# Performance work log

Hardware: AMD Instinct MI355X
Metric: run time of the kernel (lower is better)

The kernel has to match this reference:

```python
import jax, jax.numpy as jnp
import numpy as np

B, T, D, V, LMAX = 16, 512, 256, 4233, 64
NEG = -1e30  # finite 'log zero' keeps grads NaN-free


def setup_inputs() -> dict:
    key = jax.random.key(0)
    k1, k2, k3, k4 = jax.random.split(key, 4)
    hs_pad = jax.random.normal(k1, (B, T, D), dtype=jnp.float32)
    hlens = jnp.full((B,), T, dtype=jnp.int32)
    ys_pad = jax.random.randint(k2, (B, LMAX), 1, V, dtype=jnp.int32)  # blank=0 excluded
    ys_lens = jax.random.randint(k3, (B,), LMAX // 2, LMAX + 1, dtype=jnp.int32)
    W = jax.random.normal(k4, (V, D), dtype=jnp.float32) * (1.0 / np.sqrt(D))
    b = jnp.zeros((V,), dtype=jnp.float32)
    return {"hs_pad": hs_pad, "hlens": hlens, "ys_pad": ys_pad,
            "ys_lens": ys_lens, "W": W, "b": b}


def _ctc_loss_sum(logp_tbv, ext, allow, hlens, ys_lens):
    """logp_tbv: [T,B,V] log-softmax; ext: [B,S] extended labels (blank-interleaved).
    Returns sum over batch of -log p(y|x) (torch CTCLoss reduction='sum')."""
    Tn, Bn, _ = logp_tbv.shape
    S = ext.shape[1]
    # per-frame log-prob of each extended label: [T,B,S]
    lp_ext = jnp.take_along_axis(
        logp_tbv, jnp.broadcast_to(ext[None], (Tn, Bn, S)), axis=2)

    # t = 0 init: alpha[0]=lp(blank), alpha[1]=lp(y_1)
    alpha0 = jnp.full((Bn, S), NEG, dtype=logp_tbv.dtype)
    alpha0 = alpha0.at[:, 0].set(lp_ext[0, :, 0])
    alpha0 = alpha0.at[:, 1].set(lp_ext[0, :, 1])

    def step(alpha, inp):
        lp_t, t = inp  # lp_t: [B,S]
        a1 = jnp.pad(alpha[:, :-1], ((0, 0), (1, 0)), constant_values=NEG)
        a2 = jnp.pad(alpha[:, :-2], ((0, 0), (2, 0)), constant_values=NEG)
        a2 = jnp.where(allow, a2, NEG)
        new = jnp.logaddexp(jnp.logaddexp(alpha, a1), a2) + lp_t
        alpha = jnp.where((t < hlens)[:, None], new, alpha)  # freeze past hlen
        return alpha, None

    ts = jnp.arange(1, Tn, dtype=jnp.int32)
    alpha, _ = jax.lax.scan(step, alpha0, (lp_ext[1:], ts))

    last = 2 * ys_lens  # index of final blank state
    bi = jnp.arange(Bn)
    ll = jnp.logaddexp(alpha[bi, last], alpha[bi, last - 1])
    return -jnp.sum(ll)


def reference(hs_pad, hlens, ys_pad, ys_lens, W, b):
    # linear projection + log_softmax (dropout_rate=0.0 -> identity)
    logits = jnp.einsum('btd,vd->btv', hs_pad, W) + b
    logp = jax.nn.log_softmax(logits, axis=-1)          # [B,T,V]
    logp = jnp.transpose(logp, (1, 0, 2))               # [T,B,V]

    Bn, Lmax = ys_pad.shape
    S = 2 * Lmax + 1
    ext = jnp.zeros((Bn, S), dtype=ys_pad.dtype).at[:, 1::2].set(ys_pad)
    prev2 = jnp.pad(ext, ((0, 0), (2, 0)))[:, :-2]
    allow = (ext != 0) & (ext != prev2) & (jnp.arange(S) >= 2)

    loss = _ctc_loss_sum(logp, ext, allow, hlens, ys_lens)
    return loss / Bn  # module divides by ys_hat.size(1) == batch
```

## Files before the change

### kernel.cpp

```cpp
#include <hip/hip_runtime.h>

constexpr int Bn = 16;
constexpr int Tn = 512;
constexpr int Dn = 256;
constexpr int Vn = 4233;
constexpr int Vp = 4352;
constexpr int Ln = 64;
constexpr int Un = 80;
constexpr int CS = 68;
constexpr int NCB = 34;
constexpr int Mtot = Bn * Tn;

#define LN2     0.6931471805599453f
#define INV_LN2 1.4426950408889634f

typedef __attribute__((ext_vector_type(8))) short short8;
typedef __attribute__((ext_vector_type(4))) float f32x4;

__device__ __forceinline__ float lg2(float x) { return __builtin_amdgcn_logf(x); }
__device__ __forceinline__ float ex2(float x) { return __builtin_amdgcn_exp2f(x); }

__device__ __forceinline__ unsigned short cvt_bf16(float f) {
    unsigned int u = __float_as_uint(f);
    u = (u + 0x7fffu + ((u >> 16) & 1u)) >> 16;
    return (unsigned short)u;
}

__device__ __forceinline__ void gl_lds16(const void* g, void* l) {
    __builtin_amdgcn_global_load_lds(
        (const __attribute__((address_space(1))) void*)g,
        (__attribute__((address_space(3))) void*)l,
        16, 0, 0);
}

__device__ __forceinline__ double dpp_shr1_d(double v) {
    union { double d; int i[2]; } u, r;
    u.d = v;
    r.i[0] = __builtin_amdgcn_update_dpp(0, u.i[0], 0x138, 0xF, 0xF, false);
    r.i[1] = __builtin_amdgcn_update_dpp(0, u.i[1], 0x138, 0xF, 0xF, false);
    return r.d;
}

__device__ __forceinline__ int wave_imax(int v) {
    int t;
    t = __builtin_amdgcn_update_dpp(v, v, 0xB1,  0xF, 0xF, false); v = (t > v) ? t : v;
    t = __builtin_amdgcn_update_dpp(v, v, 0x4E,  0xF, 0xF, false); v = (t > v) ? t : v;
    t = __builtin_amdgcn_update_dpp(v, v, 0x141, 0xF, 0xF, false); v = (t > v) ? t : v;
    t = __builtin_amdgcn_update_dpp(v, v, 0x140, 0xF, 0xF, false); v = (t > v) ? t : v;
    int a = __builtin_amdgcn_readlane(v, 0);
    int b = __builtin_amdgcn_readlane(v, 16);
    int c = __builtin_amdgcn_readlane(v, 32);
    int d = __builtin_amdgcn_readlane(v, 48);
    int ab = (a > b) ? a : b;
    int cd = (c > d) ? c : d;
    return (ab > cd) ? ab : cd;
}

__global__ __launch_bounds__(256) void conv(
    const float* __restrict__ hs, const float* __restrict__ W,
    const float* __restrict__ bias, const int* __restrict__ ys,
    unsigned short* __restrict__ hs_b, unsigned short* __restrict__ w_b,
    float* __restrict__ gbias, float* __restrict__ out)
{
    const int gid = blockIdx.x * 256 + threadIdx.x;
    const int stride = gridDim.x * 256;
    const float4* hs4 = (const float4*)hs;
    const float4* W4  = (const float4*)W;

    if (gid == 0) out[0] = 0.0f;

    for (int i = gid; i < (Bn * Tn * Dn) / 4; i += stride) {
        float4 v = hs4[i];
        ushort4 o = make_ushort4(cvt_bf16(v.x), cvt_bf16(v.y), cvt_bf16(v.z), cvt_bf16(v.w));
        *(ushort4*)(&hs_b[i * 4]) = o;
    }
    for (int i = gid; i < Vp * (Dn / 4); i += stride) {
        int row = i >> 6;
        float4 v = make_float4(0.f, 0.f, 0.f, 0.f);
        if (row < Vn) v = W4[i];
        ushort4 o = make_ushort4(cvt_bf16(v.x), cvt_bf16(v.y), cvt_bf16(v.z), cvt_bf16(v.w));
        *(ushort4*)(&w_b[i * 4]) = o;
    }
    for (int i = gid; i < Bn * 128; i += stride) {
        int b = i >> 7;
        int u = i & 127;
        int v = (u == 0) ? 0 : ((u <= Ln) ? ys[b * Ln + u - 1] : -1);
        gbias[i] = (v >= 0) ? bias[v] : 0.0f;
    }
}

__global__ __launch_bounds__(256) void gemm_se(
    const unsigned short* __restrict__ hs_b, const unsigned short* __restrict__ w_b,
    const int* __restrict__ ys, const float* __restrict__ bias,
    const float* __restrict__ gbias, float* __restrict__ sep,
    float* __restrict__ glg2)
{
    __shared__ __align__(16) short lsA[128 * 64];
    __shared__ __align__(16) short lsB[128 * 64];

    const int tid = threadIdx.x;
    const int lane = tid & 63;
    const int w = tid >> 6;
    const int lr = lane & 15;
    const int kq = lane >> 4;
    const int m0 = blockIdx.x * 128;
    const int mw = w * 32;
    const bool gather = (blockIdx.y == NCB);
    const int b = blockIdx.x >> 2;

    const int srow = lane >> 3;
    const int scg  = (lane & 7) ^ (srow & 7);
    const int scol = scg * 8;

    const unsigned short* bptr[4];
    #pragma unroll
    for (int j = 0; j < 4; ++j) {
        int c = w * 4 + j;
        int row = c * 8 + srow;
        int v;
        if (gather) {
            if (row == 0) v = 0;
            else if (row <= Ln) v = ys[b * Ln + row - 1];
            else v = Vn + 32;
        } else {
            v = blockIdx.y * 128 + row;
        }
        bptr[j] = w_b + (size_t)v * Dn + scol;
    }

    f32x4 acc[2][8];
    #pragma unroll
    for (int mf = 0; mf < 2; ++mf)
        #pragma unroll
        for (int nf = 0; nf < 8; ++nf)
            acc[mf][nf] = (f32x4){0.f, 0.f, 0.f, 0.f};

    for (int ks = 0; ks < 4; ++ks) {
        const int k0 = ks * 64;
        __syncthreads();
        #pragma unroll
        for (int j = 0; j < 4; ++j) {
            int c = w * 4 + j;
            int row = c * 8 + srow;
            gl_lds16(hs_b + (size_t)(m0 + row) * Dn + k0 + scol, (char*)lsA + c * 1024);
            gl_lds16(bptr[j] + k0,                               (char*)lsB + c * 1024);
        }
        __syncthreads();

        #pragma unroll
        for (int sub = 0; sub < 2; ++sub) {
            short8 af[2], bf[8];
            #pragma unroll
            for (int mf = 0; mf < 2; ++mf) {
                int row = mw + mf * 16 + lr;
                int cg = (sub * 4 + kq) ^ (row & 7);
                af[mf] = *(const short8*)(&lsA[row * 64 + cg * 8]);
            }
            #pragma unroll
            for (int nf = 0; nf < 8; ++nf) {
                int row = nf * 16 + lr;
                int cg = (sub * 4 + kq) ^ (row & 7);
                bf[nf] = *(const short8*)(&lsB[row * 64 + cg * 8]);
            }
            #pragma unroll
            for (int mf = 0; mf < 2; ++mf)
                #pragma unroll
                for (int nf = 0; nf < 8; ++nf)
                    acc[mf][nf] = __builtin_amdgcn_mfma_f32_16x16x32_bf16(
                        af[mf], bf[nf], acc[mf][nf], 0, 0, 0);
        }
    }

    if (!gather) {
        const int n0 = blockIdx.y * 128;
        float bcol[8]; bool valid[8];
        #pragma unroll
        for (int nf = 0; nf < 8; ++nf) {
            int col = n0 + nf * 16 + lr;
            valid[nf] = (col < Vn);
            bcol[nf] = valid[nf] ? bias[col] : 0.0f;
        }
        #pragma unroll
        for (int mf = 0; mf < 2; ++mf) {
            #pragma unroll
            for (int r = 0; r < 4; ++r) {
                float s = 0.0f;
                #pragma unroll
                for (int nf = 0; nf < 8; ++nf)
                    if (valid[nf]) s += __expf(acc[mf][nf][r] + bcol[nf]);
                #pragma unroll
                for (int off = 1; off < 16; off <<= 1) s += __shfl_xor(s, off, 64);
                if (lr == 0)
                    sep[(size_t)blockIdx.y * Mtot + m0 + mw + mf * 16 + kq * 4 + r] = s;
            }
        }
    } else {
        #pragma unroll
        for (int mf = 0; mf < 2; ++mf) {
            #pragma unroll
            for (int nf = 0; nf < 5; ++nf) {
                int u = nf * 16 + lr;
                float gv = gbias[b * 128 + u];
                #pragma unroll
                for (int r = 0; r < 4; ++r) {
                    int g = m0 + mw + mf * 16 + kq * 4 + r;
                    glg2[(size_t)g * Un + u] = (acc[mf][nf][r] + gv) * INV_LN2;
                }
            }
        }
    }
}

__global__ __launch_bounds__(256) void ctc_fwd(
    const float* __restrict__ pmat, const float* __restrict__ sep,
    const int* __restrict__ ys, const int* __restrict__ hlens,
    const int* __restrict__ ylens, float* __restrict__ out)
{
    __shared__ __align__(16) union SMem {
        struct {
            float ls[2][64 * CS + 4];
            double shO[64], shE[64], shZ[64];
            int   shX[64];
        } c;
        struct { float wsum[4]; } r;
    } sm;

    const int tid = threadIdx.x;
    const int l = tid & 63;
    const int w = tid >> 6;

    if (blockIdx.x >= 16) {
        const int b = blockIdx.x - 16;
        const int hl = hlens[b];
        float corrAcc = 0.0f;
        #pragma unroll
        for (int j = 0; j < 2; ++j) {
            int t = tid + j * 256;
            float s = 0.0f;
            #pragma unroll
            for (int c = 0; c < NCB; ++c)
                s += sep[(size_t)c * Mtot + b * Tn + t];
            if (t < hl) corrAcc += lg2(s);
        }
        #pragma unroll
        for (int off = 1; off < 64; off <<= 1) corrAcc += __shfl_xor(corrAcc, off, 64);
        if (l == 0) sm.r.wsum[w] = corrAcc;
        __syncthreads();
        if (tid == 0)
            atomicAdd(out, (sm.r.wsum[0] + sm.r.wsum[1] + sm.r.wsum[2] + sm.r.wsum[3])
                           * (LN2 / (float)Bn));
        return;
    }

    const int b = blockIdx.x;
    const int hl = hlens[b];
    int yl  = ys[b * Ln + l];
    int ylm = (l >= 1) ? ys[b * Ln + l - 1] : -1;
    const double aF = ((l >= 1) && (yl != ylm)) ? 1.0 : 0.0;

    const float* pm = pmat + (size_t)b * Tn * Un;

    #pragma unroll
    for (int j = 0; j < 4; ++j) {
        int i = tid + j * 256;
        int tt = i >> 4, u4 = (i & 15) * 4;
        float4 v = *(const float4*)(pm + (size_t)(1 + tt) * Un + u4);
        v.x = ex2(v.x); v.y = ex2(v.y); v.z = ex2(v.z); v.w = ex2(v.w);
        *(float4*)(&sm.c.ls[0][tt * CS + u4]) = v;
    }
    if (tid < 64) sm.c.ls[0][tid * CS + 64] = ex2(pm[(size_t)(1 + tid) * Un + 64]);
    __syncthreads();

    double o = (l == 0) ? (double)ex2(pm[1]) : 0.0;
    double e = (l == 0) ? (double)ex2(pm[0]) : 0.0;
    double z = 0.0;
    int ex = 0;

    float4 r4a = make_float4(0.f,0.f,0.f,0.f), r4b = r4a, r4c = r4a, r4d = r4a;
    float r1 = 0.0f;

    double qa0, qa1, qa2, qa3, ra0, ra1, ra2, ra3;
    double qb0, qb1, qb2, qb3, rb0, rb1, rb2, rb3;
    double qc0, qc1, qc2, qc3, rc0, rc1, rc2, rc3;

#define RENORM32 do { \
        double mm = fmax(fmax(o, e), z); \
        union { double d; unsigned int ui[2]; } um; um.d = mm; \
        int kk = (int)((um.ui[1] >> 20) & 2047u) - 1023; \
        int km = wave_imax(kk); \
        o = ldexp(o, -km); e = ldexp(e, -km); z = ldexp(z, -km); \
        ex += km; \
    } while (0)

#define STEPR(qv, rv) do { \
        double an = dpp_shr1_d(o); \
        double nO = fma(aF, an, o + e) * (rv); \
        double nE = (e + an) * (qv); \
        double nZ = (z + o) * (qv); \
        o = nO; e = nE; z = nZ; \
    } while (0)

#define LDA(base) do { \
        qa0 = (double)buf[(base) * CS];       ra0 = (double)buf[(base) * CS + 1 + l]; \
        qa1 = (double)buf[((base)+1) * CS];   ra1 = (double)buf[((base)+1) * CS + 1 + l]; \
        qa2 = (double)buf[((base)+2) * CS];   ra2 = (double)buf[((base)+2) * CS + 1 + l]; \
        qa3 = (double)buf[((base)+3) * CS];   ra3 = (double)buf[((base)+3) * CS + 1 + l]; \
    } while (0)
#define LDB(base) do { \
        qb0 = (double)buf[(base) * CS];       rb0 = (double)buf[(base) * CS + 1 + l]; \
        qb1 = (double)buf[((base)+1) * CS];   rb1 = (double)buf[((base)+1) * CS + 1 + l]; \
        qb2 = (double)buf[((base)+2) * CS];   rb2 = (double)buf[((base)+2) * CS + 1 + l]; \
        qb3 = (double)buf[((base)+3) * CS];   rb3 = (double)buf[((base)+3) * CS + 1 + l]; \
    } while (0)
#define LDC(base) do { \
        qc0 = (double)buf[(base) * CS];       rc0 = (double)buf[(base) * CS + 1 + l]; \
        qc1 = (double)buf[((base)+1) * CS];   rc1 = (double)buf[((base)+1) * CS + 1 + l]; \
        qc2 = (double)buf[((base)+2) * CS];   rc2 = (double)buf[((base)+2) * CS + 1 + l]; \
        qc3 = (double)buf[((base)+3) * CS];   rc3 = (double)buf[((base)+3) * CS + 1 + l]; \
    } while (0)

#define W4A do { STEPR(qa0,ra0); STEPR(qa1,ra1); STEPR(qa2,ra2); STEPR(qa3,ra3); } while (0)
#define W4B do { STEPR(qb0,rb0); STEPR(qb1,rb1); STEPR(qb2,rb2); STEPR(qb3,rb3); } while (0)
#define W4C do { STEPR(qc0,rc0); STEPR(qc1,rc1); STEPR(qc2,rc2); STEPR(qc3,rc3); } while (0)

#define STEPS(Joff, ACT) do { \
        RENORM32; \
        double q = (double)buf[(Joff) * CS]; \
        double r = (double)buf[(Joff) * CS + 1 + l]; \
        double an = dpp_shr1_d(o); \
        double nO = fma(aF, an, o + e) * r; \
        double nE = (e + an) * q; \
        double nZ = (z + o) * q; \
        bool act = (ACT); \
        o = act ? nO : o; e = act ? nE : e; z = act ? nZ : z; \
    } while (0)

    for (int c = 0; c < 8; ++c) {
        if (c < 7) {
            const int tb = 1 + (c + 1) * 64;
            { int i = tid;       int tt = i >> 4, u4 = (i & 15) * 4;
              r4a = (tb + tt < Tn) ? *(const float4*)(pm + (size_t)(tb + tt) * Un + u4) : make_float4(0.f,0.f,0.f,0.f); }
            { int i = tid + 256; int tt = i >> 4, u4 = (i & 15) * 4;
              r4b = (tb + tt < Tn) ? *(const float4*)(pm + (size_t)(tb + tt) * Un + u4) : make_float4(0.f,0.f,0.f,0.f); }
            { int i = tid + 512; int tt = i >> 4, u4 = (i & 15) * 4;
              r4c = (tb + tt < Tn) ? *(const float4*)(pm + (size_t)(tb + tt) * Un + u4) : make_float4(0.f,0.f,0.f,0.f); }
            { int i = tid + 768; int tt = i >> 4, u4 = (i & 15) * 4;
              r4d = (tb + tt < Tn) ? *(const float4*)(pm + (size_t)(tb + tt) * Un + u4) : make_float4(0.f,0.f,0.f,0.f); }
            if (tid < 64)
                r1 = (tb + tid < Tn) ? pm[(size_t)(tb + tid) * Un + 64] : 0.0f;
        }

        const float* buf = sm.c.ls[c & 1];

        if (c < 7) {
            if (hl >= (c + 1) * 64 + 1) {
                RENORM32;
                LDA(0); LDB(4);
                LDC(8);  W4A;
                LDA(12); W4B;
                LDB(16); W4C;
                LDC(20); W4A;
                LDA(24); W4B;
                LDB(28); W4C;
                LDC(32); W4A;
                LDA(36); W4B;
                RENORM32;
                LDB(40); W4C;
                LDC(44); W4A;
                LDA(48); W4B;
                LDB(52); W4C;
                LDC(56); W4A;
                LDA(60); W4B;
                W4C;
                W4A;
            } else {
                #pragma unroll 1
                for (int j = 0; j < 64; ++j)
                    STEPS(j, (c * 64 + 1 + j) < hl);
            }
        } else {
            if (hl >= Tn) {
                RENORM32;
                LDA(0); LDB(4);
                LDC(8);  W4A;
                LDA(12); W4B;
                LDB(16); W4C;
                LDC(20); W4A;
                LDA(24); W4B;
                LDB(28); W4C;
                LDC(32); W4A;
                LDA(36); W4B;
                RENORM32;
                LDB(40); W4C;
                LDC(44); W4A;
                LDA(48); W4B;
                LDB(52); W4C;
                LDC(56); W4A;
                LDA(60); W4B;
                W4C;
                STEPR(qa0, ra0); STEPR(qa1, ra1); STEPR(qa2, ra2);
            } else {
                #pragma unroll 1
                for (int j = 0; j < 63; ++j)
                    STEPS(j, (449 + j) < hl);
            }
        }

        if (c < 7) {
            const int tb = 1 + (c + 1) * 64;
            float* dst = sm.c.ls[(c + 1) & 1];
            { int i = tid;       int tt = i >> 4, u4 = (i & 15) * 4; float4 v = r4a;
              v.x = ex2(v.x); v.y = ex2(v.y); v.z = ex2(v.z); v.w = ex2(v.w);
              if (tb + tt >= Tn) v = make_float4(0.f,0.f,0.f,0.f);
              *(float4*)(&dst[tt * CS + u4]) = v; }
            { int i = tid + 256; int tt = i >> 4, u4 = (i & 15) * 4; float4 v = r4b;
              v.x = ex2(v.x); v.y = ex2(v.y); v.z = ex2(v.z); v.w = ex2(v.w);
              if (tb + tt >= Tn) v = make_float4(0.f,0.f,0.f,0.f);
              *(float4*)(&dst[tt * CS + u4]) = v; }
            { int i = tid + 512; int tt = i >> 4, u4 = (i & 15) * 4; float4 v = r4c;
              v.x = ex2(v.x); v.y = ex2(v.y); v.z = ex2(v.z); v.w = ex2(v.w);
              if (tb + tt >= Tn) v = make_float4(0.f,0.f,0.f,0.f);
              *(float4*)(&dst[tt * CS + u4]) = v; }
            { int i = tid + 768; int tt = i >> 4, u4 = (i & 15) * 4; float4 v = r4d;
              v.x = ex2(v.x); v.y = ex2(v.y); v.z = ex2(v.z); v.w = ex2(v.w);
              if (tb + tt >= Tn) v = make_float4(0.f,0.f,0.f,0.f);
              *(float4*)(&dst[tt * CS + u4]) = v; }
            if (tid < 64)
                dst[tid * CS + 64] = (tb + tid < Tn) ? ex2(r1) : 0.0f;
        }
        __syncthreads();
    }
#undef RENORM32
#undef STEPR
#undef LDA
#undef LDB
#undef LDC
#undef W4A
#undef W4B
#undef W4C
#undef STEPS

    if (tid < 64) { sm.c.shO[l] = o; sm.c.shE[l] = e; sm.c.shZ[l] = z; sm.c.shX[l] = ex; }
    __syncthreads();

    if (tid == 0) {
        int L = ylens[b];
        double vo = sm.c.shO[L - 1]; int xo = sm.c.shX[L - 1];
        double ve; int xe;
        if (L == 64) { ve = sm.c.shZ[63]; xe = sm.c.shX[63]; }
        else         { ve = sm.c.shE[L];  xe = sm.c.shX[L]; }
        int em = (xo > xe) ? xo : xe;
        double s = ldexp(vo, xo - em) + ldexp(ve, xe - em);
        union { double d; unsigned int ui[2]; } us; us.d = s;
        int ks = (int)((us.ui[1] >> 20) & 2047u) - 1023;
        double mant = ldexp(s, -ks);
        float ll = (lg2((float)mant) + (float)(ks + em)) * LN2;
        atomicAdd(out, -ll / (float)Bn);
    }
}

extern "C" void kernel_launch(void* const* d_in, const int* in_sizes, int n_in,
                              void* d_out, int out_size, void* d_ws, size_t ws_size,
                              hipStream_t stream) {
    const float* hs    = (const float*)d_in[0];
    const int*   hlens = (const int*)d_in[1];
    const int*   ys    = (const int*)d_in[2];
    const int*   ylens = (const int*)d_in[3];
    const float* W     = (const float*)d_in[4];
    const float* bias  = (const float*)d_in[5];
    float* out = (float*)d_out;

    char* ws = (char*)d_ws;
    unsigned short* hs_b = (unsigned short*)(ws);
    unsigned short* w_b  = (unsigned short*)(ws + 4194304);
    float* glg2  = (float*)(ws + 6422528);
    float* sep   = (float*)(ws + 9043968);
    float* gbias = (float*)(ws + 10158080);

    conv<<<1024, 256, 0, stream>>>(hs, W, bias, ys, hs_b, w_b, gbias, out);
    gemm_se<<<dim3(64, NCB + 1), 256, 0, stream>>>(hs_b, w_b, ys, bias, gbias, sep, glg2);
    ctc_fwd<<<32, 256, 0, stream>>>(glg2, sep, ys, hlens, ylens, out);
}
```

Before: 117.4 us.

## Make GEMM persistent with resident A panel and double-buffered B tiles

The GEMM grid changes from 64x35 independent tiles to 256 blocks. Each block loads its full 128x256 hs panel into LDS once, then walks every fourth column tile, double-buffering the W half-tiles so the next load overlaps MFMA work. This removes the repeated reloading of the A panel and the two barriers per k-step. In exchange it uses much more LDS (about 128KB per block at one block per CU) and leaves fewer blocks to hide latency.

Result: slower. 162.2 us (+38.2%).

```diff
diff --git a/kernel.cpp b/kernel.cpp
--- a/kernel.cpp
+++ b/kernel.cpp
@@ -89,44 +89,54 @@
     }
 }
 
-__global__ __launch_bounds__(256) void gemm_se(
+__global__ __launch_bounds__(256, 1) void gemm_se(
     const unsigned short* __restrict__ hs_b, const unsigned short* __restrict__ w_b,
     const int* __restrict__ ys, const float* __restrict__ bias,
     const float* __restrict__ gbias, float* __restrict__ sep,
     float* __restrict__ glg2)
 {
-    __shared__ __align__(16) short lsA[128 * 64];
-    __shared__ __align__(16) short lsB[128 * 64];
+    __shared__ __align__(16) short lsA[128 * 256];
+    __shared__ __align__(16) short lsB0[128 * 128];
+    __shared__ __align__(16) short lsB1[128 * 128];
 
     const int tid = threadIdx.x;
     const int lane = tid & 63;
     const int w = tid >> 6;
     const int lr = lane & 15;
     const int kq = lane >> 4;
-    const int m0 = blockIdx.x * 128;
-    const int mw = w * 32;
-    const bool gather = (blockIdx.y == NCB);
-    const int b = blockIdx.x >> 2;
-
-    const int srow = lane >> 3;
-    const int scg  = (lane & 7) ^ (srow & 7);
-    const int scol = scg * 8;
-
-    const unsigned short* bptr[4];
-    #pragma unroll
-    for (int j = 0; j < 4; ++j) {
-        int c = w * 4 + j;
-        int row = c * 8 + srow;
-        int v;
-        if (gather) {
-            if (row == 0) v = 0;
-            else if (row <= Ln) v = ys[b * Ln + row - 1];
-            else v = Vn + 32;
-        } else {
-            v = blockIdx.y * 128 + row;
-        }
-        bptr[j] = w_b + (size_t)v * Dn + scol;
-    }
+
+    const int panel = blockIdx.x >> 2;
+    const int cph   = blockIdx.x & 3;
+    const int m0 = panel * 128;
+    const int b  = panel >> 2;
+
+    {
+        const int r2 = lane >> 5;
+        const int ch = lane & 31;
+        #pragma unroll
+        for (int j = 0; j < 16; ++j) {
+            int row = w * 32 + j * 2 + r2;
+            int sch = ch ^ (row & 7);
+            gl_lds16(hs_b + (size_t)(m0 + row) * Dn + sch * 8,
+                     (char*)lsA + (w * 32 + j * 2) * 512);
+        }
+    }
+
+    auto stageB = [&](int c, int kh, short* dst) {
+        const int r4 = lane >> 4;
+        const int ch = lane & 15;
+        const bool gat = (c == NCB);
+        #pragma unroll
+        for (int j = 0; j < 8; ++j) {
+            int row = w * 32 + j * 4 + r4;
+            int vr;
+            if (gat) vr = (row == 0) ? 0 : ((row <= Ln) ? ys[b * Ln + row - 1] : Vn + 32);
+            else     vr = c * 128 + row;
+            int sch = ch ^ (row & 7);
+            gl_lds16(w_b + (size_t)vr * Dn + kh * 128 + sch * 8,
+                     (char*)dst + (w * 32 + j * 4) * 256);
+        }
+    };
 
     f32x4 acc[2][8];
     #pragma unroll
@@ -135,32 +145,21 @@
         for (int nf = 0; nf < 8; ++nf)
             acc[mf][nf] = (f32x4){0.f, 0.f, 0.f, 0.f};
 
-    for (int ks = 0; ks < 4; ++ks) {
-        const int k0 = ks * 64;
-        __syncthreads();
-        #pragma unroll
-        for (int j = 0; j < 4; ++j) {
-            int c = w * 4 + j;
-            int row = c * 8 + srow;
-            gl_lds16(hs_b + (size_t)(m0 + row) * Dn + k0 + scol, (char*)lsA + c * 1024);
-            gl_lds16(bptr[j] + k0,                               (char*)lsB + c * 1024);
-        }
-        __syncthreads();
-
-        #pragma unroll
-        for (int sub = 0; sub < 2; ++sub) {
+    auto compute = [&](int kh, const short* bsrc) {
+        #pragma unroll
+        for (int ks = 0; ks < 4; ++ks) {
             short8 af[2], bf[8];
             #pragma unroll
             for (int mf = 0; mf < 2; ++mf) {
-                int row = mw + mf * 16 + lr;
-                int cg = (sub * 4 + kq) ^ (row & 7);
-                af[mf] = *(const short8*)(&lsA[row * 64 + cg * 8]);
+                int row = w * 32 + mf * 16 + lr;
+                int chk = ((kh * 4 + ks) * 4 + kq) ^ (row & 7);
+                af[mf] = *(const short8*)(&lsA[row * 256 + chk * 8]);
             }
             #pragma unroll
             for (int nf = 0; nf < 8; ++nf) {
                 int row = nf * 16 + lr;
-                int cg = (sub * 4 + kq) ^ (row & 7);
-                bf[nf] = *(const short8*)(&lsB[row * 64 + cg * 8]);
+                int chk = (ks * 4 + kq) ^ (row & 7);
+                bf[nf] = *(const short8*)(&bsrc[row * 128 + chk * 8]);
             }
             #pragma unroll
             for (int mf = 0; mf < 2; ++mf)
@@ -169,45 +168,68 @@
                     acc[mf][nf] = __builtin_amdgcn_mfma_f32_16x16x32_bf16(
                         af[mf], bf[nf], acc[mf][nf], 0, 0, 0);
         }
-    }
-
-    if (!gather) {
-        const int n0 = blockIdx.y * 128;
-        float bcol[8]; bool valid[8];
-        #pragma unroll
-        for (int nf = 0; nf < 8; ++nf) {
-            int col = n0 + nf * 16 + lr;
-            valid[nf] = (col < Vn);
-            bcol[nf] = valid[nf] ? bias[col] : 0.0f;
-        }
-        #pragma unroll
-        for (int mf = 0; mf < 2; ++mf) {
-            #pragma unroll
-            for (int r = 0; r < 4; ++r) {
-                float s = 0.0f;
-                #pragma unroll
-                for (int nf = 0; nf < 8; ++nf)
-                    if (valid[nf]) s += __expf(acc[mf][nf][r] + bcol[nf]);
-                #pragma unroll
-                for (int off = 1; off < 16; off <<= 1) s += __shfl_xor(s, off, 64);
-                if (lr == 0)
-                    sep[(size_t)blockIdx.y * Mtot + m0 + mw + mf * 16 + kq * 4 + r] = s;
-            }
-        }
-    } else {
-        #pragma unroll
-        for (int mf = 0; mf < 2; ++mf) {
-            #pragma unroll
-            for (int nf = 0; nf < 5; ++nf) {
-                int u = nf * 16 + lr;
-                float gv = gbias[b * 128 + u];
+    };
+
+    stageB(cph, 0, lsB0);
+    __syncthreads();
+
+    for (int i = 0; i < 9; ++i) {
+        const int c = cph + 4 * i;
+        if (c > NCB) break;
+
+        stageB(c, 1, lsB1);
+        compute(0, lsB0);
+        __syncthreads();
+
+        const int c2 = c + 4;
+        if (c2 <= NCB) stageB(c2, 0, lsB0);
+        compute(1, lsB1);
+
+        if (c < NCB) {
+            const int n0 = c * 128;
+            float bcol[8]; bool valid[8];
+            #pragma unroll
+            for (int nf = 0; nf < 8; ++nf) {
+                int col = n0 + nf * 16 + lr;
+                valid[nf] = (col < Vn);
+                bcol[nf] = valid[nf] ? bias[col] : 0.0f;
+            }
+            #pragma unroll
+            for (int mf = 0; mf < 2; ++mf) {
                 #pragma unroll
                 for (int r = 0; r < 4; ++r) {
-                    int g = m0 + mw + mf * 16 + kq * 4 + r;
-                    glg2[(size_t)g * Un + u] = (acc[mf][nf][r] + gv) * INV_LN2;
+                    float s = 0.0f;
+                    #pragma unroll
+                    for (int nf = 0; nf < 8; ++nf)
+                        if (valid[nf]) s += __expf(acc[mf][nf][r] + bcol[nf]);
+                    #pragma unroll
+                    for (int off = 1; off < 16; off <<= 1) s += __shfl_xor(s, off, 64);
+                    if (lr == 0)
+                        sep[(size_t)c * Mtot + m0 + w * 32 + mf * 16 + kq * 4 + r] = s;
                 }
             }
-        }
+        } else {
+            #pragma unroll
+            for (int mf = 0; mf < 2; ++mf) {
+                #pragma unroll
+                for (int nf = 0; nf < 5; ++nf) {
+                    int u = nf * 16 + lr;
+                    float gv = gbias[b * 128 + u];
+                    #pragma unroll
+                    for (int r = 0; r < 4; ++r) {
+                        int g = m0 + w * 32 + mf * 16 + kq * 4 + r;
+                        glg2[(size_t)g * Un + u] = (acc[mf][nf][r] + gv) * INV_LN2;
+                    }
+                }
+            }
+        }
+        #pragma unroll
+        for (int mf = 0; mf < 2; ++mf)
+            #pragma unroll
+            for (int nf = 0; nf < 8; ++nf)
+                acc[mf][nf] = (f32x4){0.f, 0.f, 0.f, 0.f};
+
+        __syncthreads();
     }
 }
 
@@ -478,6 +500,6 @@
     float* gbias = (float*)(ws + 10158080);
 
     conv<<<1024, 256, 0, stream>>>(hs, W, bias, ys, hs_b, w_b, gbias, out);
-    gemm_se<<<dim3(64, NCB + 1), 256, 0, stream>>>(hs_b, w_b, ys, bias, gbias, sep, glg2);
+    gemm_se<<<256, 256, 0, stream>>>(hs_b, w_b, ys, bias, gbias, sep, glg2);
     ctc_fwd<<<32, 256, 0, stream>>>(glg2, sep, ys, hlens, ylens, out);
 }
```

## Split CTC recursion into forward alpha and backward beta halves meeting mid-sequence

Applied to the files above, without the earlier changes.

The CTC recursion is split so that one block per utterance runs the forward alpha pass over the first half of the frames while a second block runs a backward beta pass over the second half. The two results are combined at the midpoint through a global workspace and an atomic pair counter: whichever block finishes second computes the dot product of alpha and beta to get the log-likelihood. This roughly halves the serial dependency chain, which dominates the CTC kernel. In exchange it adds a workspace handshake, a separate slow fallback path for hlen != T, and a more complex midpoint combine.

Result: faster. 113.8 us (-3.1%).

```diff
diff --git a/kernel.cpp b/kernel.cpp
--- a/kernel.cpp
+++ b/kernel.cpp
@@ -38,6 +38,14 @@
     u.d = v;
     r.i[0] = __builtin_amdgcn_update_dpp(0, u.i[0], 0x138, 0xF, 0xF, false);
     r.i[1] = __builtin_amdgcn_update_dpp(0, u.i[1], 0x138, 0xF, 0xF, false);
+    return r.d;
+}
+
+__device__ __forceinline__ double dpp_shl1_d(double v) {
+    union { double d; int i[2]; } u, r;
+    u.d = v;
+    r.i[0] = __builtin_amdgcn_update_dpp(0, u.i[0], 0x130, 0xF, 0xF, false);
+    r.i[1] = __builtin_amdgcn_update_dpp(0, u.i[1], 0x130, 0xF, 0xF, false);
     return r.d;
 }
 
@@ -60,7 +68,7 @@
     const float* __restrict__ hs, const float* __restrict__ W,
     const float* __restrict__ bias, const int* __restrict__ ys,
     unsigned short* __restrict__ hs_b, unsigned short* __restrict__ w_b,
-    float* __restrict__ gbias, float* __restrict__ out)
+    float* __restrict__ gbias, float* __restrict__ out, int* __restrict__ pcnt)
 {
     const int gid = blockIdx.x * 256 + threadIdx.x;
     const int stride = gridDim.x * 256;
@@ -68,6 +76,7 @@
     const float4* W4  = (const float4*)W;
 
     if (gid == 0) out[0] = 0.0f;
+    if (gid < 16) pcnt[gid] = 0;
 
     for (int i = gid; i < (Bn * Tn * Dn) / 4; i += stride) {
         float4 v = hs4[i];
@@ -214,7 +223,8 @@
 __global__ __launch_bounds__(256) void ctc_fwd(
     const float* __restrict__ pmat, const float* __restrict__ sep,
     const int* __restrict__ ys, const int* __restrict__ hlens,
-    const int* __restrict__ ylens, float* __restrict__ out)
+    const int* __restrict__ ylens, float* __restrict__ out,
+    double* __restrict__ pairws, int* __restrict__ pcnt)
 {
     __shared__ __align__(16) union SMem {
         struct {
@@ -223,14 +233,24 @@
             int   shX[64];
         } c;
         struct { float wsum[4]; } r;
+        struct { double shD[64]; int flag; } p;
     } sm;
 
     const int tid = threadIdx.x;
     const int l = tid & 63;
     const int w = tid >> 6;
 
-    if (blockIdx.x >= 16) {
-        const int b = blockIdx.x - 16;
+    double* aO = pairws;
+    double* aE = pairws + 1024;
+    double* aZ = pairws + 2048;
+    double* bOw = pairws + 3072;
+    double* bBw = pairws + 4096;
+    double* bZw = pairws + 5120;
+    int* aX = (int*)(pairws + 6144);
+    int* bX = aX + 16;
+
+    if (blockIdx.x >= 32) {
+        const int b = blockIdx.x - 32;
         const int hl = hlens[b];
         float corrAcc = 0.0f;
         #pragma unroll
@@ -252,13 +272,269 @@
         return;
     }
 
-    const int b = blockIdx.x;
+    const bool isBeta = (blockIdx.x >= 16);
+    const int b = blockIdx.x & 15;
     const int hl = hlens[b];
-    int yl  = ys[b * Ln + l];
-    int ylm = (l >= 1) ? ys[b * Ln + l - 1] : -1;
+    const float* pm = pmat + (size_t)b * Tn * Un;
+    const int yl  = ys[b * Ln + l];
+
+#define RENA do { \
+        double mm = fmax(fmax(o, e), z); \
+        union { double d; unsigned int ui[2]; } um; um.d = mm; \
+        int kk = (int)((um.ui[1] >> 20) & 2047u) - 1023; \
+        int km = wave_imax(kk); \
+        o = ldexp(o, -km); e = ldexp(e, -km); z = ldexp(z, -km); \
+        ex += km; \
+    } while (0)
+
+#define STEPR(qv, rv) do { \
+        double an = dpp_shr1_d(o); \
+        double nO = fma(aF, an, o + e) * (rv); \
+        double nE = (e + an) * (qv); \
+        double nZ = (z + o) * (qv); \
+        o = nO; e = nE; z = nZ; \
+    } while (0)
+
+#define LDA(base) do { \
+        qa0 = (double)buf[(base) * CS];       ra0 = (double)buf[(base) * CS + 1 + l]; \
+        qa1 = (double)buf[((base)+1) * CS];   ra1 = (double)buf[((base)+1) * CS + 1 + l]; \
+        qa2 = (double)buf[((base)+2) * CS];   ra2 = (double)buf[((base)+2) * CS + 1 + l]; \
+        qa3 = (double)buf[((base)+3) * CS];   ra3 = (double)buf[((base)+3) * CS + 1 + l]; \
+    } while (0)
+#define LDB(base) do { \
+        qb0 = (double)buf[(base) * CS];       rb0 = (double)buf[(base) * CS + 1 + l]; \
+        qb1 = (double)buf[((base)+1) * CS];   rb1 = (double)buf[((base)+1) * CS + 1 + l]; \
+        qb2 = (double)buf[((base)+2) * CS];   rb2 = (double)buf[((base)+2) * CS + 1 + l]; \
+        qb3 = (double)buf[((base)+3) * CS];   rb3 = (double)buf[((base)+3) * CS + 1 + l]; \
+    } while (0)
+#define LDC(base) do { \
+        qc0 = (double)buf[(base) * CS];       rc0 = (double)buf[(base) * CS + 1 + l]; \
+        qc1 = (double)buf[((base)+1) * CS];   rc1 = (double)buf[((base)+1) * CS + 1 + l]; \
+        qc2 = (double)buf[((base)+2) * CS];   rc2 = (double)buf[((base)+2) * CS + 1 + l]; \
+        qc3 = (double)buf[((base)+3) * CS];   rc3 = (double)buf[((base)+3) * CS + 1 + l]; \
+    } while (0)
+
+#define W4A do { STEPR(qa0,ra0); STEPR(qa1,ra1); STEPR(qa2,ra2); STEPR(qa3,ra3); } while (0)
+#define W4B do { STEPR(qb0,rb0); STEPR(qb1,rb1); STEPR(qb2,rb2); STEPR(qb3,rb3); } while (0)
+#define W4C do { STEPR(qc0,rc0); STEPR(qc1,rc1); STEPR(qc2,rc2); STEPR(qc3,rc3); } while (0)
+
+#define RENB do { \
+        double mm = fmax(fmax(bo, bb), bz); \
+        union { double d; unsigned int ui[2]; } um; um.d = mm; \
+        int kk = (int)((um.ui[1] >> 20) & 2047u) - 1023; \
+        int km = wave_imax(kk); \
+        bo = ldexp(bo, -km); bb = ldexp(bb, -km); bz = ldexp(bz, -km); \
+        exB += km; \
+    } while (0)
+
+#define BSTEP(qv, rv, nv) do { \
+        double an = dpp_shl1_d(bo); \
+        double t0  = fma(qv, bb, (rv) * bo); \
+        double nBb = fma(nv, an, (qv) * bb); \
+        double nBz = fma(rv, bo, (qv) * bz); \
+        bo = fma(aFn * (nv), an, t0); \
+        bb = nBb; bz = nBz; \
+    } while (0)
+
+#define BLA(base) do { \
+        qa0=(double)buf[(base)*CS];     ra0=(double)buf[(base)*CS+1+l];     na0=(double)buf[(base)*CS+2+l]; \
+        qa1=(double)buf[((base)+1)*CS]; ra1=(double)buf[((base)+1)*CS+1+l]; na1=(double)buf[((base)+1)*CS+2+l]; \
+        qa2=(double)buf[((base)+2)*CS]; ra2=(double)buf[((base)+2)*CS+1+l]; na2=(double)buf[((base)+2)*CS+2+l]; \
+        qa3=(double)buf[((base)+3)*CS]; ra3=(double)buf[((base)+3)*CS+1+l]; na3=(double)buf[((base)+3)*CS+2+l]; \
+    } while (0)
+#define BLB(base) do { \
+        qb0=(double)buf[(base)*CS];     rb0=(double)buf[(base)*CS+1+l];     nb0=(double)buf[(base)*CS+2+l]; \
+        qb1=(double)buf[((base)+1)*CS]; rb1=(double)buf[((base)+1)*CS+1+l]; nb1=(double)buf[((base)+1)*CS+2+l]; \
+        qb2=(double)buf[((base)+2)*CS]; rb2=(double)buf[((base)+2)*CS+1+l]; nb2=(double)buf[((base)+2)*CS+2+l]; \
+        qb3=(double)buf[((base)+3)*CS]; rb3=(double)buf[((base)+3)*CS+1+l]; nb3=(double)buf[((base)+3)*CS+2+l]; \
+    } while (0)
+#define BLC(base) do { \
+        qc0=(double)buf[(base)*CS];     rc0=(double)buf[(base)*CS+1+l];     nc0=(double)buf[(base)*CS+2+l]; \
+        qc1=(double)buf[((base)+1)*CS]; rc1=(double)buf[((base)+1)*CS+1+l]; nc1=(double)buf[((base)+1)*CS+2+l]; \
+        qc2=(double)buf[((base)+2)*CS]; rc2=(double)buf[((base)+2)*CS+1+l]; nc2=(double)buf[((base)+2)*CS+2+l]; \
+        qc3=(double)buf[((base)+3)*CS]; rc3=(double)buf[((base)+3)*CS+1+l]; nc3=(double)buf[((base)+3)*CS+2+l]; \
+    } while (0)
+
+#define BW4A do { BSTEP(qa0,ra0,na0); BSTEP(qa1,ra1,na1); BSTEP(qa2,ra2,na2); BSTEP(qa3,ra3,na3); } while (0)
+#define BW4B do { BSTEP(qb0,rb0,nb0); BSTEP(qb1,rb1,nb1); BSTEP(qb2,rb2,nb2); BSTEP(qb3,rb3,nb3); } while (0)
+#define BW4C do { BSTEP(qc0,rc0,nc0); BSTEP(qc1,rc1,nc1); BSTEP(qc2,rc2,nc2); BSTEP(qc3,rc3,nc3); } while (0)
+
+#define PAIR_COMBINE(myX) do { \
+        if (tid == 0) { \
+            int old = __hip_atomic_fetch_add(&pcnt[b], 1, __ATOMIC_ACQ_REL, __HIP_MEMORY_SCOPE_AGENT); \
+            sm.p.flag = (old == 1); \
+        } \
+        __syncthreads(); \
+        if (!sm.p.flag) return; \
+        __threadfence(); \
+        int pemaxv = 0; \
+        if (tid < 64) { \
+            double o_ = aO[b*64+l], e_ = aE[b*64+l], z_ = aZ[b*64+l]; \
+            double po = bOw[b*64+l], pb = bBw[b*64+l], pz = bZw[b*64+l]; \
+            int e1,e2,e3,e4,e5,e6; \
+            double m1 = frexp(o_, &e1), m2 = frexp(po, &e2); \
+            double m3 = frexp(e_, &e3), m4 = frexp(pz, &e4); \
+            double m5 = frexp(z_, &e5), m6 = frexp(pb, &e6); \
+            double q1 = m1*m2; int x1 = e1+e2; \
+            double q2 = m3*m4; int x2 = e3+e4; \
+            double q3 = (l==63) ? m5*m6 : 0.0; int x3 = e5+e6; \
+            int pe = -(1<<30); \
+            if (q1 != 0.0) pe = x1; \
+            if (q2 != 0.0 && x2 > pe) pe = x2; \
+            if (q3 != 0.0 && x3 > pe) pe = x3; \
+            pemaxv = wave_imax(pe); \
+            double cc = 0.0; \
+            if (q1 != 0.0) cc += ldexp(q1, x1 - pemaxv); \
+            if (q2 != 0.0) cc += ldexp(q2, x2 - pemaxv); \
+            if (q3 != 0.0) cc += ldexp(q3, x3 - pemaxv); \
+            sm.p.shD[l] = cc; \
+        } \
+        __syncthreads(); \
+        if (tid == 0) { \
+            double s = 0.0; \
+            for (int i2 = 0; i2 < 64; ++i2) s += sm.p.shD[i2]; \
+            int ext = aX[b] + bX[b] + pemaxv; \
+            float ll = (lg2((float)s) + (float)ext) * LN2; \
+            atomicAdd(out, -ll / (float)Bn); \
+        } \
+    } while (0)
+
+    if (isBeta) {
+        if (hl != Tn) return;
+        const int Ly = ylens[b];
+        const int yn = (l < 63) ? ys[b * Ln + l + 1] : -1;
+        const double aFn = ((l < 63) && (yn != yl)) ? 1.0 : 0.0;
+
+        #pragma unroll
+        for (int j = 0; j < 4; ++j) {
+            int i = tid + j * 256;
+            int tt = i >> 4, u4 = (i & 15) * 4;
+            float4 v = *(const float4*)(pm + (size_t)(511 - tt) * Un + u4);
+            v.x = ex2(v.x); v.y = ex2(v.y); v.z = ex2(v.z); v.w = ex2(v.w);
+            *(float4*)(&sm.c.ls[0][tt * CS + u4]) = v;
+        }
+        if (tid < 64) {
+            sm.c.ls[0][tid * CS + 64] = ex2(pm[(size_t)(511 - tid) * Un + 64]);
+            sm.c.ls[0][tid * CS + 65] = 0.0f;
+        }
+        __syncthreads();
+
+        double bo = (l == Ly - 1) ? 1.0 : 0.0;
+        double bb = (l == Ly - 1) ? 1.0 : 0.0;
+        double bz = (l == Ly)     ? 1.0 : 0.0;
+        int exB = 0;
+
+        float4 r4a = make_float4(0.f,0.f,0.f,0.f), r4b = r4a, r4c = r4a, r4d = r4a;
+        float r1 = 0.0f;
+
+        double qa0,qa1,qa2,qa3, ra0,ra1,ra2,ra3, na0,na1,na2,na3;
+        double qb0,qb1,qb2,qb3, rb0,rb1,rb2,rb3, nb0,nb1,nb2,nb3;
+        double qc0,qc1,qc2,qc3, rc0,rc1,rc2,rc3, nc0,nc1,nc2,nc3;
+
+        for (int k = 0; k < 4; ++k) {
+            if (k < 3) {
+                const int fb = 511 - (k + 1) * 64;
+                { int i = tid;       int tt = i >> 4, u4 = (i & 15) * 4;
+                  r4a = *(const float4*)(pm + (size_t)(fb - tt) * Un + u4); }
+                { int i = tid + 256; int tt = i >> 4, u4 = (i & 15) * 4;
+                  r4b = *(const float4*)(pm + (size_t)(fb - tt) * Un + u4); }
+                { int i = tid + 512; int tt = i >> 4, u4 = (i & 15) * 4;
+                  r4c = *(const float4*)(pm + (size_t)(fb - tt) * Un + u4); }
+                { int i = tid + 768; int tt = i >> 4, u4 = (i & 15) * 4;
+                  r4d = *(const float4*)(pm + (size_t)(fb - tt) * Un + u4); }
+                if (tid < 64) r1 = pm[(size_t)(fb - tid) * Un + 64];
+            }
+
+            const float* buf = sm.c.ls[k & 1];
+
+            RENB;
+            BLA(0); BLB(4);
+            BLC(8);  BW4A;
+            BLA(12); BW4B;
+            BLB(16); BW4C;
+            BLC(20); BW4A;
+            BLA(24); BW4B;
+            BLB(28); BW4C;
+            BLC(32); BW4A;
+            BLA(36); BW4B;
+            RENB;
+            BLB(40); BW4C;
+            BLC(44); BW4A;
+            BLA(48); BW4B;
+            BLB(52); BW4C;
+            BLC(56); BW4A;
+            BLA(60); BW4B;
+            BW4C;
+            BW4A;
+
+            if (k < 3) {
+                float* dst = sm.c.ls[(k + 1) & 1];
+                { int i = tid;       int tt = i >> 4, u4 = (i & 15) * 4; float4 v = r4a;
+                  v.x = ex2(v.x); v.y = ex2(v.y); v.z = ex2(v.z); v.w = ex2(v.w);
+                  *(float4*)(&dst[tt * CS + u4]) = v; }
+                { int i = tid + 256; int tt = i >> 4, u4 = (i & 15) * 4; float4 v = r4b;
+                  v.x = ex2(v.x); v.y = ex2(v.y); v.z = ex2(v.z); v.w = ex2(v.w);
+                  *(float4*)(&dst[tt * CS + u4]) = v; }
+                { int i = tid + 512; int tt = i >> 4, u4 = (i & 15) * 4; float4 v = r4c;
+                  v.x = ex2(v.x); v.y = ex2(v.y); v.z = ex2(v.z); v.w = ex2(v.w);
+                  *(float4*)(&dst[tt * CS + u4]) = v; }
+                { int i = tid + 768; int tt = i >> 4, u4 = (i & 15) * 4; float4 v = r4d;
+                  v.x = ex2(v.x); v.y = ex2(v.y); v.z = ex2(v.z); v.w = ex2(v.w);
+                  *(float4*)(&dst[tt * CS + u4]) = v; }
+                if (tid < 64) {
+                    dst[tid * CS + 64] = ex2(r1);
+                    dst[tid * CS + 65] = 0.0f;
+                }
+            }
+            __syncthreads();
+        }
+
+        if (tid < 64) { bOw[b*64+l] = bo; bBw[b*64+l] = bb; bZw[b*64+l] = bz; }
+        if (tid == 0) bX[b] = exB;
+        __threadfence();
+        __syncthreads();
+        PAIR_COMBINE(bX);
+        return;
+    }
+
+    const int ylm = (l >= 1) ? ys[b * Ln + l - 1] : -1;
     const double aF = ((l >= 1) && (yl != ylm)) ? 1.0 : 0.0;
 
-    const float* pm = pmat + (size_t)b * Tn * Un;
+    if (hl != Tn) {
+        double o = (l == 0) ? (double)ex2(pm[1]) : 0.0;
+        double e = (l == 0) ? (double)ex2(pm[0]) : 0.0;
+        double z = 0.0;
+        int ex = 0;
+        #pragma unroll 1
+        for (int t = 1; t < Tn; ++t) {
+            RENA;
+            double q = (double)ex2(pm[(size_t)t * Un]);
+            double r = (double)ex2(pm[(size_t)t * Un + 1 + l]);
+            double an = dpp_shr1_d(o);
+            double nO = fma(aF, an, o + e) * r;
+            double nE = (e + an) * q;
+            double nZ = (z + o) * q;
+            bool act = (t < hl);
+            o = act ? nO : o; e = act ? nE : e; z = act ? nZ : z;
+        }
+        if (tid < 64) { sm.c.shO[l] = o; sm.c.shE[l] = e; sm.c.shZ[l] = z; sm.c.shX[l] = ex; }
+        __syncthreads();
+        if (tid == 0) {
+            int L = ylens[b];
+            double vo = sm.c.shO[L - 1]; int xo = sm.c.shX[L - 1];
+            double ve; int xe;
+            if (L == 64) { ve = sm.c.shZ[63]; xe = sm.c.shX[63]; }
+            else         { ve = sm.c.shE[L];  xe = sm.c.shX[L]; }
+            int em = (xo > xe) ? xo : xe;
+            double s = ldexp(vo, xo - em) + ldexp(ve, xe - em);
+            union { double d; unsigned int ui[2]; } us; us.d = s;
+            int ks = (int)((us.ui[1] >> 20) & 2047u) - 1023;
+            double mant = ldexp(s, -ks);
+            float ll = (lg2((float)mant) + (float)(ks + em)) * LN2;
+            atomicAdd(out, -ll / (float)Bn);
+        }
+        return;
+    }
 
     #pragma unroll
     for (int j = 0; j < 4; ++j) {
@@ -283,154 +559,90 @@
     double qb0, qb1, qb2, qb3, rb0, rb1, rb2, rb3;
     double qc0, qc1, qc2, qc3, rc0, rc1, rc2, rc3;
 
-#define RENORM32 do { \
-        double mm = fmax(fmax(o, e), z); \
-        union { double d; unsigned int ui[2]; } um; um.d = mm; \
-        int kk = (int)((um.ui[1] >> 20) & 2047u) - 1023; \
-        int km = wave_imax(kk); \
-        o = ldexp(o, -km); e = ldexp(e, -km); z = ldexp(z, -km); \
-        ex += km; \
-    } while (0)
-
-#define STEPR(qv, rv) do { \
-        double an = dpp_shr1_d(o); \
-        double nO = fma(aF, an, o + e) * (rv); \
-        double nE = (e + an) * (qv); \
-        double nZ = (z + o) * (qv); \
-        o = nO; e = nE; z = nZ; \
-    } while (0)
-
-#define LDA(base) do { \
-        qa0 = (double)buf[(base) * CS];       ra0 = (double)buf[(base) * CS + 1 + l]; \
-        qa1 = (double)buf[((base)+1) * CS];   ra1 = (double)buf[((base)+1) * CS + 1 + l]; \
-        qa2 = (double)buf[((base)+2) * CS];   ra2 = (double)buf[((base)+2) * CS + 1 + l]; \
-        qa3 = (double)buf[((base)+3) * CS];   ra3 = (double)buf[((base)+3) * CS + 1 + l]; \
-    } while (0)
-#define LDB(base) do { \
-        qb0 = (double)buf[(base) * CS];       rb0 = (double)buf[(base) * CS + 1 + l]; \
-        qb1 = (double)buf[((base)+1) * CS];   rb1 = (double)buf[((base)+1) * CS + 1 + l]; \
-        qb2 = (double)buf[((base)+2) * CS];   rb2 = (double)buf[((base)+2) * CS + 1 + l]; \
-        qb3 = (double)buf[((base)+3) * CS];   rb3 = (double)buf[((base)+3) * CS + 1 + l]; \
-    } while (0)
-#define LDC(base) do { \
-        qc0 = (double)buf[(base) * CS];       rc0 = (double)buf[(base) * CS + 1 + l]; \
-        qc1 = (double)buf[((base)+1) * CS];   rc1 = (double)buf[((base)+1) * CS + 1 + l]; \
-        qc2 = (double)buf[((base)+2) * CS];   rc2 = (double)buf[((base)+2) * CS + 1 + l]; \
-        qc3 = (double)buf[((base)+3) * CS];   rc3 = (double)buf[((base)+3) * CS + 1 + l]; \
-    } while (0)
-
-#define W4A do { STEPR(qa0,ra0); STEPR(qa1,ra1); STEPR(qa2,ra2); STEPR(qa3,ra3); } while (0)
-#define W4B do { STEPR(qb0,rb0); STEPR(qb1,rb1); STEPR(qb2,rb2); STEPR(qb3,rb3); } while (0)
-#define W4C do { STEPR(qc0,rc0); STEPR(qc1,rc1); STEPR(qc2,rc2); STEPR(qc3,rc3); } while (0)
-
-#define STEPS(Joff, ACT) do { \
-        RENORM32; \
-        double q = (double)buf[(Joff) * CS]; \
-        double r = (double)buf[(Joff) * CS + 1 + l]; \
-        double an = dpp_shr1_d(o); \
-        double nO = fma(aF, an, o + e) * r; \
-        double nE = (e + an) * q; \
-        double nZ = (z + o) * q; \
-        bool act = (ACT); \
-        o = act ? nO : o; e = act ? nE : e; z = act ? nZ : z; \
-    } while (0)
-
-    for (int c = 0; c < 8; ++c) {
-        if (c < 7) {
+    for (int c = 0; c < 4; ++c) {
+        if (c < 3) {
             const int tb = 1 + (c + 1) * 64;
             { int i = tid;       int tt = i >> 4, u4 = (i & 15) * 4;
-              r4a = (tb + tt < Tn) ? *(const float4*)(pm + (size_t)(tb + tt) * Un + u4) : make_float4(0.f,0.f,0.f,0.f); }
+              r4a = *(const float4*)(pm + (size_t)(tb + tt) * Un + u4); }
             { int i = tid + 256; int tt = i >> 4, u4 = (i & 15) * 4;
-              r4b = (tb + tt < Tn) ? *(const float4*)(pm + (size_t)(tb + tt) * Un + u4) : make_float4(0.f,0.f,0.f,0.f); }
+              r4b = *(const float4*)(pm + (size_t)(tb + tt) * Un + u4); }
             { int i = tid + 512; int tt = i >> 4, u4 = (i & 15) * 4;
-              r4c = (tb + tt < Tn) ? *(const float4*)(pm + (size_t)(tb + tt) * Un + u4) : make_float4(0.f,0.f,0.f,0.f); }
+              r4c = *(const float4*)(pm + (size_t)(tb + tt) * Un + u4); }
             { int i = tid + 768; int tt = i >> 4, u4 = (i & 15) * 4;
-              r4d = (tb + tt < Tn) ? *(const float4*)(pm + (size_t)(tb + tt) * Un + u4) : make_float4(0.f,0.f,0.f,0.f); }
+              r4d = *(const float4*)(pm + (size_t)(tb + tt) * Un + u4); }
             if (tid < 64)
-                r1 = (tb + tid < Tn) ? pm[(size_t)(tb + tid) * Un + 64] : 0.0f;
+                r1 = pm[(size_t)(tb + tid) * Un + 64];
         }
 
         const float* buf = sm.c.ls[c & 1];
 
-        if (c < 7) {
-            if (hl >= (c + 1) * 64 + 1) {
-                RENORM32;
-                LDA(0); LDB(4);
-                LDC(8);  W4A;
-                LDA(12); W4B;
-                LDB(16); W4C;
-                LDC(20); W4A;
-                LDA(24); W4B;
-                LDB(28); W4C;
-                LDC(32); W4A;
-                LDA(36); W4B;
-                RENORM32;
-                LDB(40); W4C;
-                LDC(44); W4A;
-                LDA(48); W4B;
-                LDB(52); W4C;
-                LDC(56); W4A;
-                LDA(60); W4B;
-                W4C;
-                W4A;
-            } else {
-                #pragma unroll 1
-                for (int j = 0; j < 64; ++j)
-                    STEPS(j, (c * 64 + 1 + j) < hl);
-            }
+        if (c < 3) {
+            RENA;
+            LDA(0); LDB(4);
+            LDC(8);  W4A;
+            LDA(12); W4B;
+            LDB(16); W4C;
+            LDC(20); W4A;
+            LDA(24); W4B;
+            LDB(28); W4C;
+            LDC(32); W4A;
+            LDA(36); W4B;
+            RENA;
+            LDB(40); W4C;
+            LDC(44); W4A;
+            LDA(48); W4B;
+            LDB(52); W4C;
+            LDC(56); W4A;
+            LDA(60); W4B;
+            W4C;
+            W4A;
         } else {
-            if (hl >= Tn) {
-                RENORM32;
-                LDA(0); LDB(4);
-                LDC(8);  W4A;
-                LDA(12); W4B;
-                LDB(16); W4C;
-                LDC(20); W4A;
-                LDA(24); W4B;
-                LDB(28); W4C;
-                LDC(32); W4A;
-                LDA(36); W4B;
-                RENORM32;
-                LDB(40); W4C;
-                LDC(44); W4A;
-                LDA(48); W4B;
-                LDB(52); W4C;
-                LDC(56); W4A;
-                LDA(60); W4B;
-                W4C;
-                STEPR(qa0, ra0); STEPR(qa1, ra1); STEPR(qa2, ra2);
-            } else {
-                #pragma unroll 1
-                for (int j = 0; j < 63; ++j)
-                    STEPS(j, (449 + j) < hl);
-            }
-        }
-
-        if (c < 7) {
-            const int tb = 1 + (c + 1) * 64;
+            RENA;
+            LDA(0); LDB(4);
+            LDC(8);  W4A;
+            LDA(12); W4B;
+            LDB(16); W4C;
+            LDC(20); W4A;
+            LDA(24); W4B;
+            LDB(28); W4C;
+            LDC(32); W4A;
+            LDA(36); W4B;
+            RENA;
+            LDB(40); W4C;
+            LDC(44); W4A;
+            LDA(48); W4B;
+            LDB(52); W4C;
+            LDC(56); W4A;
+            LDA(60); W4B;
+            W4C;
+            STEPR(qa0, ra0); STEPR(qa1, ra1); STEPR(qa2, ra2);
+        }
+
+        if (c < 3) {
             float* dst = sm.c.ls[(c + 1) & 1];
             { int i = tid;       int tt = i >> 4, u4 = (i & 15) * 4; float4 v = r4a;
               v.x = ex2(v.x); v.y = ex2(v.y); v.z = ex2(v.z); v.w = ex2(v.w);
-              if (tb + tt >= Tn) v = make_float4(0.f,0.f,0.f,0.f);
               *(float4*)(&dst[tt * CS + u4]) = v; }
             { int i = tid + 256; int tt = i >> 4, u4 = (i & 15) * 4; float4 v = r4b;
               v.x = ex2(v.x); v.y = ex2(v.y); v.z = ex2(v.z); v.w = ex2(v.w);
-              if (tb + tt >= Tn) v = make_float4(0.f,0.f,0.f,0.f);
               *(float4*)(&dst[tt * CS + u4]) = v; }
             { int i = tid + 512; int tt = i >> 4, u4 = (i & 15) * 4; float4 v = r4c;
               v.x = ex2(v.x); v.y = ex2(v.y); v.z = ex2(v.z); v.w = ex2(v.w);
-              if (tb + tt >= Tn) v = make_float4(0.f,0.f,0.f,0.f);
               *(float4*)(&dst[tt * CS + u4]) = v; }
             { int i = tid + 768; int tt = i >> 4, u4 = (i & 15) * 4; float4 v = r4d;
               v.x = ex2(v.x); v.y = ex2(v.y); v.z = ex2(v.z); v.w = ex2(v.w);
-              if (tb + tt >= Tn) v = make_float4(0.f,0.f,0.f,0.f);
               *(float4*)(&dst[tt * CS + u4]) = v; }
-            if (tid < 64)
-                dst[tid * CS + 64] = (tb + tid < Tn) ? ex2(r1) : 0.0f;
+            if (tid < 64) dst[tid * CS + 64] = ex2(r1);
         }
         __syncthreads();
     }
-#undef RENORM32
+
+    if (tid < 64) { aO[b*64+l] = o; aE[b*64+l] = e; aZ[b*64+l] = z; }
+    if (tid == 0) aX[b] = ex;
+    __threadfence();
+    __syncthreads();
+    PAIR_COMBINE(aX);
+#undef RENA
 #undef STEPR
 #undef LDA
 #undef LDB
@@ -438,25 +650,15 @@
 #undef W4A
 #undef W4B
 #undef W4C
-#undef STEPS
-
-    if (tid < 64) { sm.c.shO[l] = o; sm.c.shE[l] = e; sm.c.shZ[l] = z; sm.c.shX[l] = ex; }
-    __syncthreads();
-
-    if (tid == 0) {
-        int L = ylens[b];
-        double vo = sm.c.shO[L - 1]; int xo = sm.c.shX[L - 1];
-        double ve; int xe;
-        if (L == 64) { ve = sm.c.shZ[63]; xe = sm.c.shX[63]; }
-        else         { ve = sm.c.shE[L];  xe = sm.c.shX[L]; }
-        int em = (xo > xe) ? xo : xe;
-        double s = ldexp(vo, xo - em) + ldexp(ve, xe - em);
-        union { double d; unsigned int ui[2]; } us; us.d = s;
-        int ks = (int)((us.ui[1] >> 20) & 2047u) - 1023;
-        double mant = ldexp(s, -ks);
-        float ll = (lg2((float)mant) + (float)(ks + em)) * LN2;
-        atomicAdd(out, -ll / (float)Bn);
-    }
+#undef RENB
+#undef BSTEP
+#undef BLA
+#undef BLB
+#undef BLC
+#undef BW4A
+#undef BW4B
+#undef BW4C
+#undef PAIR_COMBINE
 }
 
 extern "C" void kernel_launch(void* const* d_in, const int* in_sizes, int n_in,
@@ -476,8 +678,10 @@
     float* glg2  = (float*)(ws + 6422528);
     float* sep   = (float*)(ws + 9043968);
     float* gbias = (float*)(ws + 10158080);
-
-    conv<<<1024, 256, 0, stream>>>(hs, W, bias, ys, hs_b, w_b, gbias, out);
+    double* pairws = (double*)(ws + 10166272);
+    int*    pcnt   = (int*)(ws + 10215552);
+
+    conv<<<1024, 256, 0, stream>>>(hs, W, bias, ys, hs_b, w_b, gbias, out, pcnt);
     gemm_se<<<dim3(64, NCB + 1), 256, 0, stream>>>(hs_b, w_b, ys, bias, gbias, sep, glg2);
-    ctc_fwd<<<32, 256, 0, stream>>>(glg2, sep, ys, hlens, ylens, out);
-}
+    ctc_fwd<<<48, 256, 0, stream>>>(glg2, sep, ys, hlens, ylens, out, pairws, pcnt);
+}
```
